# Kernel optimization log

Measured on AMD Instinct MI355X. Metric: run time of the kernel, lower is better.

The kernel has to match this reference:

```python
import jax, jax.numpy as jnp
import numpy as np

B, S, H, D = 2, 2048, 16, 128

def setup_inputs() -> dict:
    key = jax.random.key(0)
    kq, kk, kv = jax.random.split(key, 3)
    q = jax.random.normal(kq, (B, S, H, D), dtype=jnp.float32)
    k = jax.random.normal(kk, (B, S, H, D), dtype=jnp.float32)
    v = jax.random.normal(kv, (B, S, H, D), dtype=jnp.float32)
    return {"q": q, "k": k, "v": v}

def reference(q, k, v):
    # Flash-attention semantics: layout [B, S, H, D], causal mask,
    # softmax_scale = 1/sqrt(head_dim), no dropout/window/alibi/bias.
    scale = 1.0 / jnp.sqrt(jnp.asarray(q.shape[-1], dtype=q.dtype))
    # scores: [B, H, Sq, Sk]
    scores = jnp.einsum("bqhd,bkhd->bhqk", q, k) * scale
    sq, sk = q.shape[1], k.shape[1]
    causal_mask = jnp.arange(sk)[None, :] <= jnp.arange(sq)[:, None]  # [Sq, Sk]
    scores = jnp.where(causal_mask[None, None, :, :], scores, jnp.finfo(scores.dtype).min)
    probs = jax.nn.softmax(scores, axis=-1)
    out = jnp.einsum("bhqk,bkhd->bqhd", probs, v)
    return out
```

## Files before the change

kernel.cpp:

```cpp
#include <hip/hip_runtime.h>
#include <hip/hip_bf16.h>

namespace {

constexpr int Bn = 2, Sn = 2048, Hn = 16, Dn = 128;
constexpr int QBLK = 128;
constexpr int KVBLK = 32;
constexpr int RS = Hn * Dn;
constexpr float QSCALE = 0.08838834764831845f * 1.4426950408889634f;

typedef __bf16 bf16x8 __attribute__((ext_vector_type(8)));
typedef __bf16 bf16x4 __attribute__((ext_vector_type(4)));
typedef float  f32x16 __attribute__((ext_vector_type(16)));

__device__ __forceinline__ f32x16 mfma32(bf16x8 a, bf16x8 b, f32x16 c) {
  return __builtin_amdgcn_mfma_f32_32x32x16_bf16(a, b, c, 0, 0, 0);
}
__device__ __forceinline__ unsigned pack2(float a, float b) {
  union { __bf16 h[2]; unsigned u; } r;
  r.h[0] = (__bf16)a; r.h[1] = (__bf16)b;
  return r.u;
}
__device__ __forceinline__ float pair_max(float x, int hi) {
  auto r = __builtin_amdgcn_permlane32_swap(__float_as_uint(x), __float_as_uint(x), false, false);
  const float sw = __uint_as_float(hi ? r[0] : r[1]);
  return fmaxf(x, sw);
}
__device__ __forceinline__ float pair_sum(float x, int hi) {
  auto r = __builtin_amdgcn_permlane32_swap(__float_as_uint(x), __float_as_uint(x), false, false);
  const float sw = __uint_as_float(hi ? r[0] : r[1]);
  return x + sw;
}
__device__ __forceinline__ float f4e(const float4& v, int j) {
  return j == 0 ? v.x : j == 1 ? v.y : j == 2 ? v.z : v.w;
}
__device__ __forceinline__ float lane_bcast(int row, float v) {
  return __uint_as_float(__builtin_amdgcn_ds_bpermute(row * 4, __float_as_uint(v)));
}

__device__ __forceinline__ void pipeline_barrier() {
  __builtin_amdgcn_sched_barrier(0);
  asm volatile("s_waitcnt lgkmcnt(0)" ::: "memory");
  __builtin_amdgcn_s_barrier();
  __builtin_amdgcn_sched_barrier(0);
}

__global__ __launch_bounds__(512)
void fa_fwd(const float* __restrict__ Q, const float* __restrict__ K,
            const float* __restrict__ V, float* __restrict__ O)
{
  __shared__ __align__(16) __bf16 Klds[6][KVBLK * 128];
  __shared__ __align__(16) __bf16 Vt[4][128 * KVBLK];

  const int tid  = threadIdx.x;
  const int lane = tid & 63;
  const int wave = tid >> 6;
  const int col  = lane & 31;
  const int hi   = lane >> 5;
  const int grp  = wave >> 2;
  const int wq   = wave & 3;

  const int xcd  = (int)blockIdx.x & 7;
  const int s    = (int)blockIdx.x >> 3;
  const int hidx = xcd * 4 + (s & 3);
  const int b    = hidx >> 4, h = hidx & 15;
  const int s2   = s >> 2;
  const int qt   = (s < 32) ? (15 - s2) : (s2 - 8);
  const int q0w  = qt * QBLK + wq * 32;
  const int T    = 2 * (qt + 1);
  const size_t base = ((size_t)b * Sn) * RS + (size_t)h * Dn;

  const int sthalf = tid >> 8, ht = tid & 255;
  const int skey = ht >> 3, sd = (ht & 7) * 16;
  const int vkey4 = (ht & 7) * 4, vd4 = (ht >> 3) * 4;

  float4 kr[4], vr[4];
  auto loadK = [&](int ss) {
    const int kv0 = (2 * ss + sthalf) * KVBLK;
    const float* kp = K + base + (size_t)(kv0 + skey) * RS + sd;
#pragma unroll
    for (int i = 0; i < 4; ++i) kr[i] = *(const float4*)(kp + 4 * i);
  };
  auto loadV = [&](int ss) {
    const int kv0 = (2 * ss + sthalf) * KVBLK;
    const float* vp = V + base + (size_t)(kv0 + vkey4) * RS + vd4;
#pragma unroll
    for (int i = 0; i < 4; ++i) vr[i] = *(const float4*)(vp + (size_t)i * RS);
  };
  auto stageK = [&](int ss) {
    char* kb = (char*)&Klds[(2 * ss + sthalf) % 6][0];
    const int kbase = skey * 256 + sd * 2;
    const int kswz  = (skey & 7) << 4;
#pragma unroll
    for (int i = 0; i < 2; ++i) {
      bf16x8 f;
      f[0] = (__bf16)kr[2*i].x;   f[1] = (__bf16)kr[2*i].y;
      f[2] = (__bf16)kr[2*i].z;   f[3] = (__bf16)kr[2*i].w;
      f[4] = (__bf16)kr[2*i+1].x; f[5] = (__bf16)kr[2*i+1].y;
      f[6] = (__bf16)kr[2*i+1].z; f[7] = (__bf16)kr[2*i+1].w;
      *(bf16x8*)(kb + ((kbase + 16 * i) ^ kswz)) = f;
    }
  };
  auto stageV = [&](int ss) {
    char* vb = (char*)&Vt[(2 * ss + sthalf) & 3][0];
    const int b6 = ((vd4 >> 3) & 1) << 6;
#pragma unroll
    for (int j = 0; j < 4; ++j) {
      bf16x4 w;
      w[0] = (__bf16)f4e(vr[0], j);
      w[1] = (__bf16)f4e(vr[1], j);
      w[2] = (__bf16)f4e(vr[2], j);
      w[3] = (__bf16)f4e(vr[3], j);
      const int addr = (((vd4 + j) * 64 + vkey4 * 2) ^ (j << 4)) ^ b6;
      *(bf16x4*)(vb + addr) = w;
    }
  };

  const int cswz = (col & 7) << 4;
  const int vswz = ((col & 3) << 4) ^ (((col >> 3) & 1) << 6);

  bf16x8 qf[8];
  {
    const float* qp = Q + base + (size_t)(q0w + col) * RS + hi * 8;
#pragma unroll
    for (int kk = 0; kk < 8; ++kk) {
      float4 a = *(const float4*)(qp + kk * 16);
      float4 c2 = *(const float4*)(qp + kk * 16 + 4);
      bf16x8 f;
      f[0] = (__bf16)(a.x * QSCALE);  f[1] = (__bf16)(a.y * QSCALE);
      f[2] = (__bf16)(a.z * QSCALE);  f[3] = (__bf16)(a.w * QSCALE);
      f[4] = (__bf16)(c2.x * QSCALE); f[5] = (__bf16)(c2.y * QSCALE);
      f[6] = (__bf16)(c2.z * QSCALE); f[7] = (__bf16)(c2.w * QSCALE);
      qf[kk] = f;
    }
  }

  f32x16 o0 = {}, o1 = {}, o2 = {}, o3 = {};
  float m = -1e30f, l = 0.f;

  loadK(0); loadV(0);
  stageK(0);
  loadK(1);
  stageV(0);
  loadV(1);
  stageK(1);
  if (2 < T) loadK(2);
  pipeline_barrier();

  f32x16 st_cur = {};
  if (grp * KVBLK <= q0w + 31) {
    const char* kb = (const char*)&Klds[grp][0];
    __builtin_amdgcn_s_setprio(1);
#pragma unroll
    for (int kk = 0; kk < 8; ++kk) {
      bf16x8 ka = *(const bf16x8*)(kb + ((col * 256 + kk * 32 + hi * 16) ^ cswz));
      st_cur = mfma32(ka, qf[kk], st_cur);
    }
    __builtin_amdgcn_s_setprio(0);
  }

#pragma unroll 1
  for (int t = 0; t < T; ++t) {
    f32x16 stn = {};
    const int icn = 2 * (t + 1) + grp;
    if (t + 1 < T && icn * KVBLK <= q0w + 31) {
      const char* kb = (const char*)&Klds[icn % 6][0];
      __builtin_amdgcn_s_setprio(1);
#pragma unroll
      for (int kk = 0; kk < 8; ++kk) {
        bf16x8 ka = *(const bf16x8*)(kb + ((col * 256 + kk * 32 + hi * 16) ^ cswz));
        stn = mfma32(ka, qf[kk], stn);
      }
      __builtin_amdgcn_s_setprio(0);
    }

    if (t + 2 < T) stageK(t + 2);
    if (t + 1 < T) stageV(t + 1);
    if (t + 3 < T) loadK(t + 3);
    if (t + 2 < T) loadV(t + 2);

    const int kv0 = (2 * t + grp) * KVBLK;
    if (kv0 <= q0w + 31) {
      if (kv0 + KVBLK - 1 > q0w) {
        const int qk = q0w + col - kv0;
#pragma unroll
        for (int r = 0; r < 16; ++r) {
          const int krow = (r & 3) + 8 * (r >> 2) + 4 * hi;
          st_cur[r] = (krow <= qk) ? st_cur[r] : -1e30f;
        }
      }

      float t8[8];
#pragma unroll
      for (int r = 0; r < 8; ++r) t8[r] = fmaxf(st_cur[r], st_cur[r + 8]);
#pragma unroll
      for (int r = 0; r < 4; ++r) t8[r] = fmaxf(t8[r], t8[r + 4]);
      const float pmax = pair_max(fmaxf(fmaxf(t8[0], t8[1]), fmaxf(t8[2], t8[3])), hi);

      if (!__all(pmax <= m + 11.0f)) {
        const float mnew = fmaxf(m, pmax);
        const float al = __builtin_amdgcn_exp2f(m - mnew);
        m = mnew;
        l *= al;
#pragma unroll
        for (int r = 0; r < 16; ++r) {
          const int row = (r & 3) + 8 * (r >> 2) + 4 * hi;
          const float ar = lane_bcast(row, al);
          o0[r] *= ar; o1[r] *= ar; o2[r] *= ar; o3[r] *= ar;
        }
      }

      float s4[4] = {0.f, 0.f, 0.f, 0.f};
#pragma unroll
      for (int r = 0; r < 16; ++r) {
        st_cur[r] = __builtin_amdgcn_exp2f(st_cur[r] - m);
        s4[r & 3] += st_cur[r];
      }
      l += pair_sum((s4[0] + s4[1]) + (s4[2] + s4[3]), hi);

      unsigned cw[8];
#pragma unroll
      for (int i = 0; i < 8; ++i) cw[i] = pack2(st_cur[2 * i], st_cur[2 * i + 1]);
      union { unsigned u[4]; bf16x8 v; } pa0, pa1;
      {
        auto s02 = __builtin_amdgcn_permlane32_swap(cw[0], cw[2], false, false);
        auto s13 = __builtin_amdgcn_permlane32_swap(cw[1], cw[3], false, false);
        auto s46 = __builtin_amdgcn_permlane32_swap(cw[4], cw[6], false, false);
        auto s57 = __builtin_amdgcn_permlane32_swap(cw[5], cw[7], false, false);
        pa0.u[0] = s02[0]; pa0.u[2] = s02[1];
        pa0.u[1] = s13[0]; pa0.u[3] = s13[1];
        pa1.u[0] = s46[0]; pa1.u[2] = s46[1];
        pa1.u[1] = s57[0]; pa1.u[3] = s57[1];
      }

      const char* vb = (const char*)&Vt[(2 * t + grp) & 3][0];
      __builtin_amdgcn_s_setprio(1);
#pragma unroll
      for (int ks = 0; ks < 2; ++ks) {
        const bf16x8 pa = ks ? pa1.v : pa0.v;
#define PV_STEP(ovar, dt) { \
        bf16x8 vf = *(const bf16x8*)(vb + ((((dt)*32 + col) * 64 + ks * 32 + hi * 16) ^ vswz)); \
        ovar = mfma32(pa, vf, ovar); }
        PV_STEP(o0, 0) PV_STEP(o1, 1) PV_STEP(o2, 2) PV_STEP(o3, 3)
#undef PV_STEP
      }
      __builtin_amdgcn_s_setprio(0);
    }
    pipeline_barrier();
    st_cur = stn;
  }

  float* ob  = reinterpret_cast<float*>(&Klds[0][0]);
  float* mlb = reinterpret_cast<float*>(&Vt[0][0]);
  if (grp == 1) {
    mlb[wq * 128 + lane] = m;
    mlb[wq * 128 + 64 + lane] = l;
#pragma unroll
    for (int r = 0; r < 16; ++r) {
      ob[wq * 1024 + r * 64 + lane] = o0[r];
      ob[4096 + wq * 1024 + r * 64 + lane] = o1[r];
    }
  }
  __syncthreads();
  float f0 = 1.f, f1 = 0.f;
  if (grp == 0) {
    const float m1 = mlb[wq * 128 + lane];
    const float l1 = mlb[wq * 128 + 64 + lane];
    const float mS = fmaxf(m, m1);
    f0 = __builtin_amdgcn_exp2f(m - mS);
    f1 = __builtin_amdgcn_exp2f(m1 - mS);
    l = l * f0 + l1 * f1;
#pragma unroll
    for (int r = 0; r < 16; ++r) {
      const int row = (r & 3) + 8 * (r >> 2) + 4 * hi;
      const float a0 = lane_bcast(row, f0), a1 = lane_bcast(row, f1);
      o0[r] = o0[r] * a0 + ob[wq * 1024 + r * 64 + lane] * a1;
      o1[r] = o1[r] * a0 + ob[4096 + wq * 1024 + r * 64 + lane] * a1;
    }
  }
  __syncthreads();
  if (grp == 1) {
#pragma unroll
    for (int r = 0; r < 16; ++r) {
      ob[wq * 1024 + r * 64 + lane] = o2[r];
      ob[4096 + wq * 1024 + r * 64 + lane] = o3[r];
    }
  }
  __syncthreads();
  if (grp == 0) {
#pragma unroll
    for (int r = 0; r < 16; ++r) {
      const int row = (r & 3) + 8 * (r >> 2) + 4 * hi;
      const float a0 = lane_bcast(row, f0), a1 = lane_bcast(row, f1);
      o2[r] = o2[r] * a0 + ob[wq * 1024 + r * 64 + lane] * a1;
      o3[r] = o3[r] * a0 + ob[4096 + wq * 1024 + r * 64 + lane] * a1;
    }
    const float linv = 1.0f / l;
#pragma unroll
    for (int r = 0; r < 16; ++r) {
      const int row = (r & 3) + 8 * (r >> 2) + 4 * hi;
      const float lr = lane_bcast(row, linv);
      float* op = O + base + (size_t)(q0w + row) * RS + col;
      op[0]  = o0[r] * lr;
      op[32] = o1[r] * lr;
      op[64] = o2[r] * lr;
      op[96] = o3[r] * lr;
    }
  }
}

}

extern "C" void kernel_launch(void* const* d_in, const int* , int ,
                              void* d_out, int , void* , size_t ,
                              hipStream_t stream) {
  const float* q = (const float*)d_in[0];
  const float* k = (const float*)d_in[1];
  const float* v = (const float*)d_in[2];
  float* o = (float*)d_out;
  dim3 grid(Bn * Hn * (Sn / QBLK));
  dim3 blk(512);
  hipLaunchKernelGGL(fa_fwd, grid, blk, 0, stream, q, k, v, o);
}
```

Baseline: 104.2 us.

## Pre-convert K/V to swizzled bf16 images and stream them via direct-to-LDS loads

Adds a prep kernel that converts K and V to bf16, pre-swizzled and with V transposed, into a workspace buffer. The attention kernel then stages tiles with global_load_lds 16-byte copies straight into LDS, replacing the register load, convert and LDS store path, and waits on vmcnt at each barrier. This halves the bytes the attention kernel reads for K/V and frees VALU and registers, at the cost of an extra kernel launch and a full fp32 read plus bf16 write of K/V. The original kernel is kept as a fallback when the workspace is missing or too small.

```diff
diff --git a/kernel.cpp b/kernel.cpp
--- a/kernel.cpp
+++ b/kernel.cpp
@@ -9,6 +9,9 @@
 constexpr int RS = Hn * Dn;
 constexpr float QSCALE = 0.08838834764831845f * 1.4426950408889634f;
 
+constexpr size_t IMG_BYTES = (size_t)Bn * Hn * 64 * 8192;
+constexpr size_t WS_NEED   = 2 * IMG_BYTES;
+
 typedef __bf16 bf16x8 __attribute__((ext_vector_type(8)));
 typedef __bf16 bf16x4 __attribute__((ext_vector_type(4)));
 typedef float  f32x16 __attribute__((ext_vector_type(16)));
@@ -38,6 +41,18 @@
   return __uint_as_float(__builtin_amdgcn_ds_bpermute(row * 4, __float_as_uint(v)));
 }
 
+__device__ __forceinline__ void cp16(const char* g, char* l) {
+  __builtin_amdgcn_global_load_lds(
+      (const __attribute__((address_space(1))) void*)g,
+      (__attribute__((address_space(3))) void*)l, 16, 0, 0);
+}
+
+__device__ __forceinline__ void dma_barrier() {
+  __builtin_amdgcn_sched_barrier(0);
+  asm volatile("s_waitcnt vmcnt(0) lgkmcnt(0)" ::: "memory");
+  __builtin_amdgcn_s_barrier();
+  __builtin_amdgcn_sched_barrier(0);
+}
 __device__ __forceinline__ void pipeline_barrier() {
   __builtin_amdgcn_sched_barrier(0);
   asm volatile("s_waitcnt lgkmcnt(0)" ::: "memory");
@@ -45,12 +60,44 @@
   __builtin_amdgcn_sched_barrier(0);
 }
 
+__global__ __launch_bounds__(256)
+void prep_kv(const float* __restrict__ K, const float* __restrict__ V,
+             __bf16* __restrict__ KI, __bf16* __restrict__ VI)
+{
+  const int gid  = (int)blockIdx.x * 256 + (int)threadIdx.x;
+  const int half = gid >> 20;
+  const int id   = gid & ((1 << 20) - 1);
+  const int chunk = id >> 9;
+  const int rem   = id & 511;
+  const int bh = chunk >> 6, c = chunk & 63;
+  const int b = bh >> 4, h = bh & 15;
+  if (half == 0) {
+    const int key = rem >> 4, dblk = rem & 15;
+    const float* src = K + ((size_t)b * Sn + (size_t)c * 32 + key) * RS + h * Dn + dblk * 8;
+    float4 a  = *(const float4*)src;
+    float4 c2 = *(const float4*)(src + 4);
+    bf16x8 f;
+    f[0] = (__bf16)a.x;  f[1] = (__bf16)a.y;  f[2] = (__bf16)a.z;  f[3] = (__bf16)a.w;
+    f[4] = (__bf16)c2.x; f[5] = (__bf16)c2.y; f[6] = (__bf16)c2.z; f[7] = (__bf16)c2.w;
+    char* dst = (char*)KI + (size_t)chunk * 8192 + ((key * 256 + dblk * 16) ^ ((key & 7) << 4));
+    *(bf16x8*)dst = f;
+  } else {
+    const int d = rem >> 2, koct = rem & 3;
+    const float* src = V + ((size_t)b * Sn + (size_t)c * 32 + koct * 8) * RS + h * Dn + d;
+    bf16x8 f;
+#pragma unroll
+    for (int j = 0; j < 8; ++j) f[j] = (__bf16)src[(size_t)j * RS];
+    const int off = (d * 64 + koct * 16) ^ ((d & 3) << 4) ^ (((d >> 3) & 1) << 6);
+    *(bf16x8*)((char*)VI + (size_t)chunk * 8192 + off) = f;
+  }
+}
+
 __global__ __launch_bounds__(512)
-void fa_fwd(const float* __restrict__ Q, const float* __restrict__ K,
-            const float* __restrict__ V, float* __restrict__ O)
+void fa_fwd_dma(const float* __restrict__ Q, const __bf16* __restrict__ KI,
+                const __bf16* __restrict__ VI, float* __restrict__ O)
 {
-  __shared__ __align__(16) __bf16 Klds[6][KVBLK * 128];
-  __shared__ __align__(16) __bf16 Vt[4][128 * KVBLK];
+  __shared__ __align__(16) __bf16 Klds[4][4096];
+  __shared__ __align__(16) __bf16 Vt[4][4096];
 
   const int tid  = threadIdx.x;
   const int lane = tid & 63;
@@ -70,49 +117,27 @@
   const int T    = 2 * (qt + 1);
   const size_t base = ((size_t)b * Sn) * RS + (size_t)h * Dn;
 
-  const int sthalf = tid >> 8, ht = tid & 255;
-  const int skey = ht >> 3, sd = (ht & 7) * 16;
-  const int vkey4 = (ht & 7) * 4, vd4 = (ht >> 3) * 4;
-
-  float4 kr[4], vr[4];
-  auto loadK = [&](int ss) {
-    const int kv0 = (2 * ss + sthalf) * KVBLK;
-    const float* kp = K + base + (size_t)(kv0 + skey) * RS + sd;
-#pragma unroll
-    for (int i = 0; i < 4; ++i) kr[i] = *(const float4*)(kp + 4 * i);
+  const char* KIc = (const char*)KI + (size_t)hidx * 64 * 8192;
+  const char* VIc = (const char*)VI + (size_t)hidx * 64 * 8192;
+
+  const int sr = wave >> 1;
+  const int hb = (wave & 1) * 4096;
+  auto stageK2 = [&](int ss) {
+    if (sr < 2) {
+      const int ck = 2 * ss + sr;
+      const char* g = KIc + (size_t)ck * 8192 + hb;
+      char* l = (char*)&Klds[ck & 3][0] + hb;
+#pragma unroll
+      for (int i = 0; i < 4; ++i) cp16(g + i * 1024 + lane * 16, l + i * 1024);
+    }
   };
-  auto loadV = [&](int ss) {
-    const int kv0 = (2 * ss + sthalf) * KVBLK;
-    const float* vp = V + base + (size_t)(kv0 + vkey4) * RS + vd4;
-#pragma unroll
-    for (int i = 0; i < 4; ++i) vr[i] = *(const float4*)(vp + (size_t)i * RS);
-  };
-  auto stageK = [&](int ss) {
-    char* kb = (char*)&Klds[(2 * ss + sthalf) % 6][0];
-    const int kbase = skey * 256 + sd * 2;
-    const int kswz  = (skey & 7) << 4;
-#pragma unroll
-    for (int i = 0; i < 2; ++i) {
-      bf16x8 f;
-      f[0] = (__bf16)kr[2*i].x;   f[1] = (__bf16)kr[2*i].y;
-      f[2] = (__bf16)kr[2*i].z;   f[3] = (__bf16)kr[2*i].w;
-      f[4] = (__bf16)kr[2*i+1].x; f[5] = (__bf16)kr[2*i+1].y;
-      f[6] = (__bf16)kr[2*i+1].z; f[7] = (__bf16)kr[2*i+1].w;
-      *(bf16x8*)(kb + ((kbase + 16 * i) ^ kswz)) = f;
-    }
-  };
-  auto stageV = [&](int ss) {
-    char* vb = (char*)&Vt[(2 * ss + sthalf) & 3][0];
-    const int b6 = ((vd4 >> 3) & 1) << 6;
-#pragma unroll
-    for (int j = 0; j < 4; ++j) {
-      bf16x4 w;
-      w[0] = (__bf16)f4e(vr[0], j);
-      w[1] = (__bf16)f4e(vr[1], j);
-      w[2] = (__bf16)f4e(vr[2], j);
-      w[3] = (__bf16)f4e(vr[3], j);
-      const int addr = (((vd4 + j) * 64 + vkey4 * 2) ^ (j << 4)) ^ b6;
-      *(bf16x4*)(vb + addr) = w;
+  auto stageV2 = [&](int ss) {
+    if (sr >= 2) {
+      const int cv = 2 * ss + (sr - 2);
+      const char* g = VIc + (size_t)cv * 8192 + hb;
+      char* l = (char*)&Vt[cv & 3][0] + hb;
+#pragma unroll
+      for (int i = 0; i < 4; ++i) cp16(g + i * 1024 + lane * 16, l + i * 1024);
     }
   };
 
@@ -138,14 +163,10 @@
   f32x16 o0 = {}, o1 = {}, o2 = {}, o3 = {};
   float m = -1e30f, l = 0.f;
 
-  loadK(0); loadV(0);
-  stageK(0);
-  loadK(1);
-  stageV(0);
-  loadV(1);
-  stageK(1);
-  if (2 < T) loadK(2);
-  pipeline_barrier();
+  stageK2(0);
+  stageV2(0);
+  stageK2(1);
+  dma_barrier();
 
   f32x16 st_cur = {};
   if (grp * KVBLK <= q0w + 31) {
@@ -158,13 +179,17 @@
     }
     __builtin_amdgcn_s_setprio(0);
   }
+  dma_barrier();
 
 #pragma unroll 1
   for (int t = 0; t < T; ++t) {
+    if (t + 2 < T) stageK2(t + 2);
+    if (t + 1 < T) stageV2(t + 1);
+
     f32x16 stn = {};
     const int icn = 2 * (t + 1) + grp;
     if (t + 1 < T && icn * KVBLK <= q0w + 31) {
-      const char* kb = (const char*)&Klds[icn % 6][0];
+      const char* kb = (const char*)&Klds[icn & 3][0];
       __builtin_amdgcn_s_setprio(1);
 #pragma unroll
       for (int kk = 0; kk < 8; ++kk) {
@@ -173,11 +198,6 @@
       }
       __builtin_amdgcn_s_setprio(0);
     }
-
-    if (t + 2 < T) stageK(t + 2);
-    if (t + 1 < T) stageV(t + 1);
-    if (t + 3 < T) loadK(t + 3);
-    if (t + 2 < T) loadV(t + 2);
 
     const int kv0 = (2 * t + grp) * KVBLK;
     if (kv0 <= q0w + 31) {
@@ -246,7 +266,7 @@
       }
       __builtin_amdgcn_s_setprio(0);
     }
-    pipeline_barrier();
+    dma_barrier();
     st_cur = stn;
   }
 
@@ -309,16 +329,285 @@
   }
 }
 
+__global__ __launch_bounds__(512)
+void fa_fwd_reg(const float* __restrict__ Q, const float* __restrict__ K,
+                const float* __restrict__ V, float* __restrict__ O)
+{
+  __shared__ __align__(16) __bf16 Klds[6][KVBLK * 128];
+  __shared__ __align__(16) __bf16 Vt[4][128 * KVBLK];
+
+  const int tid  = threadIdx.x;
+  const int lane = tid & 63;
+  const int wave = tid >> 6;
+  const int col  = lane & 31;
+  const int hi   = lane >> 5;
+  const int grp  = wave >> 2;
+  const int wq   = wave & 3;
+
+  const int xcd  = (int)blockIdx.x & 7;
+  const int s    = (int)blockIdx.x >> 3;
+  const int hidx = xcd * 4 + (s & 3);
+  const int b    = hidx >> 4, h = hidx & 15;
+  const int s2   = s >> 2;
+  const int qt   = (s < 32) ? (15 - s2) : (s2 - 8);
+  const int q0w  = qt * QBLK + wq * 32;
+  const int T    = 2 * (qt + 1);
+  const size_t base = ((size_t)b * Sn) * RS + (size_t)h * Dn;
+
+  const int sthalf = tid >> 8, ht = tid & 255;
+  const int skey = ht >> 3, sd = (ht & 7) * 16;
+  const int vkey4 = (ht & 7) * 4, vd4 = (ht >> 3) * 4;
+
+  float4 kr[4], vr[4];
+  auto loadK = [&](int ss) {
+    const int kv0 = (2 * ss + sthalf) * KVBLK;
+    const float* kp = K + base + (size_t)(kv0 + skey) * RS + sd;
+#pragma unroll
+    for (int i = 0; i < 4; ++i) kr[i] = *(const float4*)(kp + 4 * i);
+  };
+  auto loadV = [&](int ss) {
+    const int kv0 = (2 * ss + sthalf) * KVBLK;
+    const float* vp = V + base + (size_t)(kv0 + vkey4) * RS + vd4;
+#pragma unroll
+    for (int i = 0; i < 4; ++i) vr[i] = *(const float4*)(vp + (size_t)i * RS);
+  };
+  auto stageK = [&](int ss) {
+    char* kb = (char*)&Klds[(2 * ss + sthalf) % 6][0];
+    const int kbase = skey * 256 + sd * 2;
+    const int kswz  = (skey & 7) << 4;
+#pragma unroll
+    for (int i = 0; i < 2; ++i) {
+      bf16x8 f;
+      f[0] = (__bf16)kr[2*i].x;   f[1] = (__bf16)kr[2*i].y;
+      f[2] = (__bf16)kr[2*i].z;   f[3] = (__bf16)kr[2*i].w;
+      f[4] = (__bf16)kr[2*i+1].x; f[5] = (__bf16)kr[2*i+1].y;
+      f[6] = (__bf16)kr[2*i+1].z; f[7] = (__bf16)kr[2*i+1].w;
+      *(bf16x8*)(kb + ((kbase + 16 * i) ^ kswz)) = f;
+    }
+  };
+  auto stageV = [&](int ss) {
+    char* vb = (char*)&Vt[(2 * ss + sthalf) & 3][0];
+    const int b6 = ((vd4 >> 3) & 1) << 6;
+#pragma unroll
+    for (int j = 0; j < 4; ++j) {
+      bf16x4 w;
+      w[0] = (__bf16)f4e(vr[0], j);
+      w[1] = (__bf16)f4e(vr[1], j);
+      w[2] = (__bf16)f4e(vr[2], j);
+      w[3] = (__bf16)f4e(vr[3], j);
+      const int addr = (((vd4 + j) * 64 + vkey4 * 2) ^ (j << 4)) ^ b6;
+      *(bf16x4*)(vb + addr) = w;
+    }
+  };
+
+  const int cswz = (col & 7) << 4;
+  const int vswz = ((col & 3) << 4) ^ (((col >> 3) & 1) << 6);
+
+  bf16x8 qf[8];
+  {
+    const float* qp = Q + base + (size_t)(q0w + col) * RS + hi * 8;
+#pragma unroll
+    for (int kk = 0; kk < 8; ++kk) {
+      float4 a = *(const float4*)(qp + kk * 16);
+      float4 c2 = *(const float4*)(qp + kk * 16 + 4);
+      bf16x8 f;
+      f[0] = (__bf16)(a.x * QSCALE);  f[1] = (__bf16)(a.y * QSCALE);
+      f[2] = (__bf16)(a.z * QSCALE);  f[3] = (__bf16)(a.w * QSCALE);
+      f[4] = (__bf16)(c2.x * QSCALE); f[5] = (__bf16)(c2.y * QSCALE);
+      f[6] = (__bf16)(c2.z * QSCALE); f[7] = (__bf16)(c2.w * QSCALE);
+      qf[kk] = f;
+    }
+  }
+
+  f32x16 o0 = {}, o1 = {}, o2 = {}, o3 = {};
+  float m = -1e30f, l = 0.f;
+
+  loadK(0); loadV(0);
+  stageK(0);
+  loadK(1);
+  stageV(0);
+  loadV(1);
+  stageK(1);
+  if (2 < T) loadK(2);
+  pipeline_barrier();
+
+  f32x16 st_cur = {};
+  if (grp * KVBLK <= q0w + 31) {
+    const char* kb = (const char*)&Klds[grp][0];
+    __builtin_amdgcn_s_setprio(1);
+#pragma unroll
+    for (int kk = 0; kk < 8; ++kk) {
+      bf16x8 ka = *(const bf16x8*)(kb + ((col * 256 + kk * 32 + hi * 16) ^ cswz));
+      st_cur = mfma32(ka, qf[kk], st_cur);
+    }
+    __builtin_amdgcn_s_setprio(0);
+  }
+
+#pragma unroll 1
+  for (int t = 0; t < T; ++t) {
+    f32x16 stn = {};
+    const int icn = 2 * (t + 1) + grp;
+    if (t + 1 < T && icn * KVBLK <= q0w + 31) {
+      const char* kb = (const char*)&Klds[icn % 6][0];
+      __builtin_amdgcn_s_setprio(1);
+#pragma unroll
+      for (int kk = 0; kk < 8; ++kk) {
+        bf16x8 ka = *(const bf16x8*)(kb + ((col * 256 + kk * 32 + hi * 16) ^ cswz));
+        stn = mfma32(ka, qf[kk], stn);
+      }
+      __builtin_amdgcn_s_setprio(0);
+    }
+
+    if (t + 2 < T) stageK(t + 2);
+    if (t + 1 < T) stageV(t + 1);
+    if (t + 3 < T) loadK(t + 3);
+    if (t + 2 < T) loadV(t + 2);
+
+    const int kv0 = (2 * t + grp) * KVBLK;
+    if (kv0 <= q0w + 31) {
+      if (kv0 + KVBLK - 1 > q0w) {
+        const int qk = q0w + col - kv0;
+#pragma unroll
+        for (int r = 0; r < 16; ++r) {
+          const int krow = (r & 3) + 8 * (r >> 2) + 4 * hi;
+          st_cur[r] = (krow <= qk) ? st_cur[r] : -1e30f;
+        }
+      }
+
+      float t8[8];
+#pragma unroll
+      for (int r = 0; r < 8; ++r) t8[r] = fmaxf(st_cur[r], st_cur[r + 8]);
+#pragma unroll
+      for (int r = 0; r < 4; ++r) t8[r] = fmaxf(t8[r], t8[r + 4]);
+      const float pmax = pair_max(fmaxf(fmaxf(t8[0], t8[1]), fmaxf(t8[2], t8[3])), hi);
+
+      if (!__all(pmax <= m + 11.0f)) {
+        const float mnew = fmaxf(m, pmax);
+        const float al = __builtin_amdgcn_exp2f(m - mnew);
+        m = mnew;
+        l *= al;
+#pragma unroll
+        for (int r = 0; r < 16; ++r) {
+          const int row = (r & 3) + 8 * (r >> 2) + 4 * hi;
+          const float ar = lane_bcast(row, al);
+          o0[r] *= ar; o1[r] *= ar; o2[r] *= ar; o3[r] *= ar;
+        }
+      }
+
+      float s4[4] = {0.f, 0.f, 0.f, 0.f};
+#pragma unroll
+      for (int r = 0; r < 16; ++r) {
+        st_cur[r] = __builtin_amdgcn_exp2f(st_cur[r] - m);
+        s4[r & 3] += st_cur[r];
+      }
+      l += pair_sum((s4[0] + s4[1]) + (s4[2] + s4[3]), hi);
+
+      unsigned cw[8];
+#pragma unroll
+      for (int i = 0; i < 8; ++i) cw[i] = pack2(st_cur[2 * i], st_cur[2 * i + 1]);
+      union { unsigned u[4]; bf16x8 v; } pa0, pa1;
+      {
+        auto s02 = __builtin_amdgcn_permlane32_swap(cw[0], cw[2], false, false);
+        auto s13 = __builtin_amdgcn_permlane32_swap(cw[1], cw[3], false, false);
+        auto s46 = __builtin_amdgcn_permlane32_swap(cw[4], cw[6], false, false);
+        auto s57 = __builtin_amdgcn_permlane32_swap(cw[5], cw[7], false, false);
+        pa0.u[0] = s02[0]; pa0.u[2] = s02[1];
+        pa0.u[1] = s13[0]; pa0.u[3] = s13[1];
+        pa1.u[0] = s46[0]; pa1.u[2] = s46[1];
+        pa1.u[1] = s57[0]; pa1.u[3] = s57[1];
+      }
+
+      const char* vb = (const char*)&Vt[(2 * t + grp) & 3][0];
+      __builtin_amdgcn_s_setprio(1);
+#pragma unroll
+      for (int ks = 0; ks < 2; ++ks) {
+        const bf16x8 pa = ks ? pa1.v : pa0.v;
+#define PV_STEP(ovar, dt) { \
+        bf16x8 vf = *(const bf16x8*)(vb + ((((dt)*32 + col) * 64 + ks * 32 + hi * 16) ^ vswz)); \
+        ovar = mfma32(pa, vf, ovar); }
+        PV_STEP(o0, 0) PV_STEP(o1, 1) PV_STEP(o2, 2) PV_STEP(o3, 3)
+#undef PV_STEP
+      }
+      __builtin_amdgcn_s_setprio(0);
+    }
+    pipeline_barrier();
+    st_cur = stn;
+  }
+
+  float* ob  = reinterpret_cast<float*>(&Klds[0][0]);
+  float* mlb = reinterpret_cast<float*>(&Vt[0][0]);
+  if (grp == 1) {
+    mlb[wq * 128 + lane] = m;
+    mlb[wq * 128 + 64 + lane] = l;
+#pragma unroll
+    for (int r = 0; r < 16; ++r) {
+      ob[wq * 1024 + r * 64 + lane] = o0[r];
+      ob[4096 + wq * 1024 + r * 64 + lane] = o1[r];
+    }
+  }
+  __syncthreads();
+  float f0 = 1.f, f1 = 0.f;
+  if (grp == 0) {
+    const float m1 = mlb[wq * 128 + lane];
+    const float l1 = mlb[wq * 128 + 64 + lane];
+    const float mS = fmaxf(m, m1);
+    f0 = __builtin_amdgcn_exp2f(m - mS);
+    f1 = __builtin_amdgcn_exp2f(m1 - mS);
+    l = l * f0 + l1 * f1;
+#pragma unroll
+    for (int r = 0; r < 16; ++r) {
+      const int row = (r & 3) + 8 * (r >> 2) + 4 * hi;
+      const float a0 = lane_bcast(row, f0), a1 = lane_bcast(row, f1);
+      o0[r] = o0[r] * a0 + ob[wq * 1024 + r * 64 + lane] * a1;
+      o1[r] = o1[r] * a0 + ob[4096 + wq * 1024 + r * 64 + lane] * a1;
+    }
+  }
+  __syncthreads();
+  if (grp == 1) {
+#pragma unroll
+    for (int r = 0; r < 16; ++r) {
+      ob[wq * 1024 + r * 64 + lane] = o2[r];
+      ob[4096 + wq * 1024 + r * 64 + lane] = o3[r];
+    }
+  }
+  __syncthreads();
+  if (grp == 0) {
+#pragma unroll
+    for (int r = 0; r < 16; ++r) {
+      const int row = (r & 3) + 8 * (r >> 2) + 4 * hi;
+      const float a0 = lane_bcast(row, f0), a1 = lane_bcast(row, f1);
+      o2[r] = o2[r] * a0 + ob[wq * 1024 + r * 64 + lane] * a1;
+      o3[r] = o3[r] * a0 + ob[4096 + wq * 1024 + r * 64 + lane] * a1;
+    }
+    const float linv = 1.0f / l;
+#pragma unroll
+    for (int r = 0; r < 16; ++r) {
+      const int row = (r & 3) + 8 * (r >> 2) + 4 * hi;
+      const float lr = lane_bcast(row, linv);
+      float* op = O + base + (size_t)(q0w + row) * RS + col;
+      op[0]  = o0[r] * lr;
+      op[32] = o1[r] * lr;
+      op[64] = o2[r] * lr;
+      op[96] = o3[r] * lr;
+    }
+  }
+}
+
 }
 
 extern "C" void kernel_launch(void* const* d_in, const int* , int ,
-                              void* d_out, int , void* , size_t ,
+                              void* d_out, int , void* d_ws, size_t ws_size,
                               hipStream_t stream) {
   const float* q = (const float*)d_in[0];
   const float* k = (const float*)d_in[1];
   const float* v = (const float*)d_in[2];
   float* o = (float*)d_out;
-  dim3 grid(Bn * Hn * (Sn / QBLK));
-  dim3 blk(512);
-  hipLaunchKernelGGL(fa_fwd, grid, blk, 0, stream, q, k, v, o);
-}
+  if (d_ws != nullptr && ws_size >= WS_NEED) {
+    __bf16* ki = (__bf16*)d_ws;
+    __bf16* vi = (__bf16*)((char*)d_ws + IMG_BYTES);
+    hipLaunchKernelGGL(prep_kv, dim3(8192), dim3(256), 0, stream, k, v, ki, vi);
+    hipLaunchKernelGGL(fa_fwd_dma, dim3(512), dim3(512), 0, stream, q, ki, vi, o);
+  } else {
+    hipLaunchKernelGGL(fa_fwd_reg, dim3(512), dim3(512), 0, stream, q, k, v, o);
+  }
+}
```

After: 102.3 us. Within noise of the previous version (-1.8%).

## Pre-convert K/V to swizzled bf16 images and DMA them into LDS

Applied to the files above, without the earlier changes.

Adds a prep kernel that converts K and V from fp32 to bf16 once, in the swizzled and transposed LDS layout, and writes them to workspace. The attention kernel then copies these images straight into LDS with global_load_lds instead of loading fp32 into registers and converting per block. It also drops from 8 waves split across two KV groups to 4 waves walking all KV tiles, which removes the cross-group softmax merge epilogue. The cost is an extra kernel launch and a full K/V read and write pass, plus less intra-block parallelism per query tile.

```diff
diff --git a/kernel.cpp b/kernel.cpp
--- a/kernel.cpp
+++ b/kernel.cpp
@@ -9,8 +9,10 @@
 constexpr int RS = Hn * Dn;
 constexpr float QSCALE = 0.08838834764831845f * 1.4426950408889634f;
 
+constexpr size_t IMG_BYTES = (size_t)Bn * Hn * 64 * 8192;
+constexpr size_t WS_NEED   = 2 * IMG_BYTES;
+
 typedef __bf16 bf16x8 __attribute__((ext_vector_type(8)));
-typedef __bf16 bf16x4 __attribute__((ext_vector_type(4)));
 typedef float  f32x16 __attribute__((ext_vector_type(16)));
 
 __device__ __forceinline__ f32x16 mfma32(bf16x8 a, bf16x8 b, f32x16 c) {
@@ -31,89 +33,93 @@
   const float sw = __uint_as_float(hi ? r[0] : r[1]);
   return x + sw;
 }
-__device__ __forceinline__ float f4e(const float4& v, int j) {
-  return j == 0 ? v.x : j == 1 ? v.y : j == 2 ? v.z : v.w;
-}
 __device__ __forceinline__ float lane_bcast(int row, float v) {
   return __uint_as_float(__builtin_amdgcn_ds_bpermute(row * 4, __float_as_uint(v)));
 }
 
-__device__ __forceinline__ void pipeline_barrier() {
+__device__ __forceinline__ void cp16(const char* g, char* l) {
+  __builtin_amdgcn_global_load_lds(
+      (const __attribute__((address_space(1))) void*)g,
+      (__attribute__((address_space(3))) void*)l, 16, 0, 0);
+}
+
+__device__ __forceinline__ void dma_barrier() {
   __builtin_amdgcn_sched_barrier(0);
-  asm volatile("s_waitcnt lgkmcnt(0)" ::: "memory");
+  asm volatile("s_waitcnt vmcnt(0) lgkmcnt(0)" ::: "memory");
   __builtin_amdgcn_s_barrier();
   __builtin_amdgcn_sched_barrier(0);
 }
 
-__global__ __launch_bounds__(512)
-void fa_fwd(const float* __restrict__ Q, const float* __restrict__ K,
-            const float* __restrict__ V, float* __restrict__ O)
+__global__ __launch_bounds__(256)
+void prep_kv(const float* __restrict__ K, const float* __restrict__ V,
+             __bf16* __restrict__ KI, __bf16* __restrict__ VI)
 {
-  __shared__ __align__(16) __bf16 Klds[6][KVBLK * 128];
-  __shared__ __align__(16) __bf16 Vt[4][128 * KVBLK];
+  const int gid  = (int)blockIdx.x * 256 + (int)threadIdx.x;
+  const int half = gid >> 20;
+  const int id   = gid & ((1 << 20) - 1);
+  const int chunk = id >> 9;
+  const int rem   = id & 511;
+  const int bh = chunk >> 6, c = chunk & 63;
+  const int b = bh >> 4, h = bh & 15;
+  if (half == 0) {
+    const int key = rem >> 4, dblk = rem & 15;
+    const float* src = K + ((size_t)b * Sn + (size_t)c * 32 + key) * RS + h * Dn + dblk * 8;
+    float4 a  = *(const float4*)src;
+    float4 c2 = *(const float4*)(src + 4);
+    bf16x8 f;
+    f[0] = (__bf16)a.x;  f[1] = (__bf16)a.y;  f[2] = (__bf16)a.z;  f[3] = (__bf16)a.w;
+    f[4] = (__bf16)c2.x; f[5] = (__bf16)c2.y; f[6] = (__bf16)c2.z; f[7] = (__bf16)c2.w;
+    char* dst = (char*)KI + (size_t)chunk * 8192 + ((key * 256 + dblk * 16) ^ ((key & 7) << 4));
+    *(bf16x8*)dst = f;
+  } else {
+    const int d = rem >> 2, koct = rem & 3;
+    const float* src = V + ((size_t)b * Sn + (size_t)c * 32 + koct * 8) * RS + h * Dn + d;
+    bf16x8 f;
+#pragma unroll
+    for (int j = 0; j < 8; ++j) f[j] = (__bf16)src[(size_t)j * RS];
+    const int off = (d * 64 + koct * 16) ^ ((d & 3) << 4) ^ (((d >> 3) & 1) << 6);
+    *(bf16x8*)((char*)VI + (size_t)chunk * 8192 + off) = f;
+  }
+}
+
+__global__ __launch_bounds__(256)
+void fa_fwd_w4(const float* __restrict__ Q, const __bf16* __restrict__ KI,
+               const __bf16* __restrict__ VI, float* __restrict__ O)
+{
+  __shared__ __align__(16) __bf16 Klds[4][4096];
+  __shared__ __align__(16) __bf16 Vt[4][4096];
 
   const int tid  = threadIdx.x;
   const int lane = tid & 63;
   const int wave = tid >> 6;
   const int col  = lane & 31;
   const int hi   = lane >> 5;
-  const int grp  = wave >> 2;
-  const int wq   = wave & 3;
-
-  const int xcd  = (int)blockIdx.x & 7;
-  const int s    = (int)blockIdx.x >> 3;
-  const int hidx = xcd * 4 + (s & 3);
+
+  const int xcd = (int)blockIdx.x & 7;
+  const int s   = (int)blockIdx.x >> 3;
+  const int i   = s & 7;
+  const int h2  = (s & 31) >> 3;
+  const int qt  = (s < 32) ? (15 - i) : i;
+  const int hidx = xcd * 4 + h2;
   const int b    = hidx >> 4, h = hidx & 15;
-  const int s2   = s >> 2;
-  const int qt   = (s < 32) ? (15 - s2) : (s2 - 8);
-  const int q0w  = qt * QBLK + wq * 32;
-  const int T    = 2 * (qt + 1);
+  const int q0w  = qt * QBLK + wave * 32;
+  const int T    = 4 * (qt + 1);
   const size_t base = ((size_t)b * Sn) * RS + (size_t)h * Dn;
 
-  const int sthalf = tid >> 8, ht = tid & 255;
-  const int skey = ht >> 3, sd = (ht & 7) * 16;
-  const int vkey4 = (ht & 7) * 4, vd4 = (ht >> 3) * 4;
-
-  float4 kr[4], vr[4];
-  auto loadK = [&](int ss) {
-    const int kv0 = (2 * ss + sthalf) * KVBLK;
-    const float* kp = K + base + (size_t)(kv0 + skey) * RS + sd;
-#pragma unroll
-    for (int i = 0; i < 4; ++i) kr[i] = *(const float4*)(kp + 4 * i);
+  const char* KIc = (const char*)KI + (size_t)hidx * 64 * 8192;
+  const char* VIc = (const char*)VI + (size_t)hidx * 64 * 8192;
+
+  auto stageK = [&](int c) {
+    const char* g = KIc + (size_t)c * 8192 + wave * 2048 + lane * 16;
+    char* l = (char*)&Klds[c & 3][0] + wave * 2048;
+    cp16(g, l);
+    cp16(g + 1024, l + 1024);
   };
-  auto loadV = [&](int ss) {
-    const int kv0 = (2 * ss + sthalf) * KVBLK;
-    const float* vp = V + base + (size_t)(kv0 + vkey4) * RS + vd4;
-#pragma unroll
-    for (int i = 0; i < 4; ++i) vr[i] = *(const float4*)(vp + (size_t)i * RS);
-  };
-  auto stageK = [&](int ss) {
-    char* kb = (char*)&Klds[(2 * ss + sthalf) % 6][0];
-    const int kbase = skey * 256 + sd * 2;
-    const int kswz  = (skey & 7) << 4;
-#pragma unroll
-    for (int i = 0; i < 2; ++i) {
-      bf16x8 f;
-      f[0] = (__bf16)kr[2*i].x;   f[1] = (__bf16)kr[2*i].y;
-      f[2] = (__bf16)kr[2*i].z;   f[3] = (__bf16)kr[2*i].w;
-      f[4] = (__bf16)kr[2*i+1].x; f[5] = (__bf16)kr[2*i+1].y;
-      f[6] = (__bf16)kr[2*i+1].z; f[7] = (__bf16)kr[2*i+1].w;
-      *(bf16x8*)(kb + ((kbase + 16 * i) ^ kswz)) = f;
-    }
-  };
-  auto stageV = [&](int ss) {
-    char* vb = (char*)&Vt[(2 * ss + sthalf) & 3][0];
-    const int b6 = ((vd4 >> 3) & 1) << 6;
-#pragma unroll
-    for (int j = 0; j < 4; ++j) {
-      bf16x4 w;
-      w[0] = (__bf16)f4e(vr[0], j);
-      w[1] = (__bf16)f4e(vr[1], j);
-      w[2] = (__bf16)f4e(vr[2], j);
-      w[3] = (__bf16)f4e(vr[3], j);
-      const int addr = (((vd4 + j) * 64 + vkey4 * 2) ^ (j << 4)) ^ b6;
-      *(bf16x4*)(vb + addr) = w;
-    }
+  auto stageV = [&](int c) {
+    const char* g = VIc + (size_t)c * 8192 + wave * 2048 + lane * 16;
+    char* l = (char*)&Vt[c & 3][0] + wave * 2048;
+    cp16(g, l);
+    cp16(g + 1024, l + 1024);
   };
 
   const int cswz = (col & 7) << 4;
@@ -138,18 +144,14 @@
   f32x16 o0 = {}, o1 = {}, o2 = {}, o3 = {};
   float m = -1e30f, l = 0.f;
 
-  loadK(0); loadV(0);
   stageK(0);
-  loadK(1);
   stageV(0);
-  loadV(1);
   stageK(1);
-  if (2 < T) loadK(2);
-  pipeline_barrier();
+  dma_barrier();
 
   f32x16 st_cur = {};
-  if (grp * KVBLK <= q0w + 31) {
-    const char* kb = (const char*)&Klds[grp][0];
+  {
+    const char* kb = (const char*)&Klds[0][0];
     __builtin_amdgcn_s_setprio(1);
 #pragma unroll
     for (int kk = 0; kk < 8; ++kk) {
@@ -161,10 +163,12 @@
 
 #pragma unroll 1
   for (int t = 0; t < T; ++t) {
+    if (t + 2 < T) stageK(t + 2);
+    if (t + 1 < T) stageV(t + 1);
+
     f32x16 stn = {};
-    const int icn = 2 * (t + 1) + grp;
-    if (t + 1 < T && icn * KVBLK <= q0w + 31) {
-      const char* kb = (const char*)&Klds[icn % 6][0];
+    if (t + 1 < T && 32 * (t + 1) <= q0w + 31) {
+      const char* kb = (const char*)&Klds[(t + 1) & 3][0];
       __builtin_amdgcn_s_setprio(1);
 #pragma unroll
       for (int kk = 0; kk < 8; ++kk) {
@@ -174,12 +178,7 @@
       __builtin_amdgcn_s_setprio(0);
     }
 
-    if (t + 2 < T) stageK(t + 2);
-    if (t + 1 < T) stageV(t + 1);
-    if (t + 3 < T) loadK(t + 3);
-    if (t + 2 < T) loadV(t + 2);
-
-    const int kv0 = (2 * t + grp) * KVBLK;
+    const int kv0 = 32 * t;
     if (kv0 <= q0w + 31) {
       if (kv0 + KVBLK - 1 > q0w) {
         const int qk = q0w + col - kv0;
@@ -220,7 +219,7 @@
 
       unsigned cw[8];
 #pragma unroll
-      for (int i = 0; i < 8; ++i) cw[i] = pack2(st_cur[2 * i], st_cur[2 * i + 1]);
+      for (int ii = 0; ii < 8; ++ii) cw[ii] = pack2(st_cur[2 * ii], st_cur[2 * ii + 1]);
       union { unsigned u[4]; bf16x8 v; } pa0, pa1;
       {
         auto s02 = __builtin_amdgcn_permlane32_swap(cw[0], cw[2], false, false);
@@ -233,7 +232,7 @@
         pa1.u[1] = s57[0]; pa1.u[3] = s57[1];
       }
 
-      const char* vb = (const char*)&Vt[(2 * t + grp) & 3][0];
+      const char* vb = (const char*)&Vt[t & 3][0];
       __builtin_amdgcn_s_setprio(1);
 #pragma unroll
       for (int ks = 0; ks < 2; ++ks) {
@@ -246,79 +245,34 @@
       }
       __builtin_amdgcn_s_setprio(0);
     }
-    pipeline_barrier();
+    dma_barrier();
     st_cur = stn;
   }
 
-  float* ob  = reinterpret_cast<float*>(&Klds[0][0]);
-  float* mlb = reinterpret_cast<float*>(&Vt[0][0]);
-  if (grp == 1) {
-    mlb[wq * 128 + lane] = m;
-    mlb[wq * 128 + 64 + lane] = l;
-#pragma unroll
-    for (int r = 0; r < 16; ++r) {
-      ob[wq * 1024 + r * 64 + lane] = o0[r];
-      ob[4096 + wq * 1024 + r * 64 + lane] = o1[r];
-    }
-  }
-  __syncthreads();
-  float f0 = 1.f, f1 = 0.f;
-  if (grp == 0) {
-    const float m1 = mlb[wq * 128 + lane];
-    const float l1 = mlb[wq * 128 + 64 + lane];
-    const float mS = fmaxf(m, m1);
-    f0 = __builtin_amdgcn_exp2f(m - mS);
-    f1 = __builtin_amdgcn_exp2f(m1 - mS);
-    l = l * f0 + l1 * f1;
-#pragma unroll
-    for (int r = 0; r < 16; ++r) {
-      const int row = (r & 3) + 8 * (r >> 2) + 4 * hi;
-      const float a0 = lane_bcast(row, f0), a1 = lane_bcast(row, f1);
-      o0[r] = o0[r] * a0 + ob[wq * 1024 + r * 64 + lane] * a1;
-      o1[r] = o1[r] * a0 + ob[4096 + wq * 1024 + r * 64 + lane] * a1;
-    }
-  }
-  __syncthreads();
-  if (grp == 1) {
-#pragma unroll
-    for (int r = 0; r < 16; ++r) {
-      ob[wq * 1024 + r * 64 + lane] = o2[r];
-      ob[4096 + wq * 1024 + r * 64 + lane] = o3[r];
-    }
-  }
-  __syncthreads();
-  if (grp == 0) {
-#pragma unroll
-    for (int r = 0; r < 16; ++r) {
-      const int row = (r & 3) + 8 * (r >> 2) + 4 * hi;
-      const float a0 = lane_bcast(row, f0), a1 = lane_bcast(row, f1);
-      o2[r] = o2[r] * a0 + ob[wq * 1024 + r * 64 + lane] * a1;
-      o3[r] = o3[r] * a0 + ob[4096 + wq * 1024 + r * 64 + lane] * a1;
-    }
-    const float linv = 1.0f / l;
-#pragma unroll
-    for (int r = 0; r < 16; ++r) {
-      const int row = (r & 3) + 8 * (r >> 2) + 4 * hi;
-      const float lr = lane_bcast(row, linv);
-      float* op = O + base + (size_t)(q0w + row) * RS + col;
-      op[0]  = o0[r] * lr;
-      op[32] = o1[r] * lr;
-      op[64] = o2[r] * lr;
-      op[96] = o3[r] * lr;
-    }
+  const float linv = 1.0f / l;
+#pragma unroll
+  for (int r = 0; r < 16; ++r) {
+    const int row = (r & 3) + 8 * (r >> 2) + 4 * hi;
+    const float lr = lane_bcast(row, linv);
+    float* op = O + base + (size_t)(q0w + row) * RS + col;
+    op[0]  = o0[r] * lr;
+    op[32] = o1[r] * lr;
+    op[64] = o2[r] * lr;
+    op[96] = o3[r] * lr;
   }
 }
 
 }
 
 extern "C" void kernel_launch(void* const* d_in, const int* , int ,
-                              void* d_out, int , void* , size_t ,
+                              void* d_out, int , void* d_ws, size_t ,
                               hipStream_t stream) {
   const float* q = (const float*)d_in[0];
   const float* k = (const float*)d_in[1];
   const float* v = (const float*)d_in[2];
   float* o = (float*)d_out;
-  dim3 grid(Bn * Hn * (Sn / QBLK));
-  dim3 blk(512);
-  hipLaunchKernelGGL(fa_fwd, grid, blk, 0, stream, q, k, v, o);
-}
+  __bf16* ki = (__bf16*)d_ws;
+  __bf16* vi = (__bf16*)((char*)d_ws + IMG_BYTES);
+  hipLaunchKernelGGL(prep_kv, dim3(8192), dim3(256), 0, stream, k, v, ki, vi);
+  hipLaunchKernelGGL(fa_fwd_w4, dim3(512), dim3(256), 0, stream, q, ki, vi, o);
+}
```

Result: slower. 159.3 us (+52.9%).
